# Kernel optimization log

Measured on AMD Instinct MI355X. Metric: run time of the kernel, lower is better.

The kernel has to match this reference:

```python
import jax, jax.numpy as jnp
import numpy as np


def gcn_conv(x, src, dst, W, b, num_nodes):
    # PyG GCNConv with add_self_loops=True, symmetric normalization.
    # src/dst already include self-loops.
    ones = jnp.ones(src.shape[0], dtype=x.dtype)
    deg = jax.ops.segment_sum(ones, dst, num_segments=num_nodes)  # [N]
    dinv = jnp.where(deg > 0, jax.lax.rsqrt(deg), 0.0)
    norm = dinv[src] * dinv[dst]                                   # [E+N]
    h = x @ W                                                      # [N, out]
    msg = h[src] * norm[:, None]                                   # gather + scale
    out = jax.ops.segment_sum(msg, dst, num_segments=num_nodes)    # scatter-add
    return out + b


def setup_inputs() -> dict:
    key = jax.random.key(0)
    k1, k2, k3, k4 = jax.random.split(key, 4)
    N, E = 50000, 1600000
    IN, HID, OUT = 1536, 256, 128
    x = jax.random.normal(k1, (N, IN), dtype=jnp.float32)
    edge_index = jax.random.randint(k2, (2, E), 0, N, dtype=jnp.int64)
    # Glorot-style scaled weights
    W1 = jax.random.normal(k3, (IN, HID), dtype=jnp.float32) / np.sqrt(IN)
    W2 = jax.random.normal(k4, (HID, OUT), dtype=jnp.float32) / np.sqrt(HID)
    b1 = jnp.zeros((HID,), dtype=jnp.float32)
    b2 = jnp.zeros((OUT,), dtype=jnp.float32)
    return {"x": x, "edge_index": edge_index, "W1": W1, "b1": b1,
            "W2": W2, "b2": b2, "num_nodes": N}


def reference(x, edge_index, W1, b1, W2, b2, num_nodes):
    loop = jnp.arange(num_nodes, dtype=edge_index.dtype)
    src = jnp.concatenate([edge_index[0], loop])
    dst = jnp.concatenate([edge_index[1], loop])
    h = gcn_conv(x, src, dst, W1, b1, num_nodes)
    h = jax.nn.relu(h)
    h = gcn_conv(h, src, dst, W2, b2, num_nodes)
    # F.normalize(h, dim=1): x / max(||x||_2, 1e-12)
    nrm = jnp.linalg.norm(h, axis=1, keepdims=True)
    return h / jnp.maximum(nrm, 1e-12)
```

## Files before the change

kernel.cpp:

```cpp
#include <hip/hip_runtime.h>

typedef __attribute__((ext_vector_type(4))) float f32x4;
typedef __attribute__((ext_vector_type(2))) float f32x2;
typedef __attribute__((ext_vector_type(8))) short s16x8;

static __device__ __forceinline__ unsigned short f2bf(float f) {
  unsigned int u = __builtin_bit_cast(unsigned int, f);
  u += 0x7fffu + ((u >> 16) & 1u);
  return (unsigned short)(u >> 16);
}

__global__ void zero_k(int* p, int n) {
  int i = blockIdx.x * 256 + threadIdx.x;
  if (i < n) p[i] = 0;
}
__global__ void deg_count_k(const int* __restrict__ edges, int* cnt, int E) {
  int e = blockIdx.x * 256 + threadIdx.x;
  if (e < E) atomicAdd(&cnt[edges[E + e]], 1);
}
__global__ void dinv_k(const int* __restrict__ cnt, float* dinv, int N) {
  int i = blockIdx.x * 256 + threadIdx.x;
  if (i < N) dinv[i] = rsqrtf((float)(cnt[i] + 1));
}

__global__ __launch_bounds__(256) void scan1_k(const int* __restrict__ cnt,
                                               int* __restrict__ loc,
                                               int* __restrict__ bsum, int N) {
  int t = threadIdx.x;
  int i0 = blockIdx.x * 1024 + t * 4;
  int c[4];
#pragma unroll
  for (int j = 0; j < 4; ++j) c[j] = (i0 + j < N) ? cnt[i0 + j] : 0;
  int tsum = c[0] + c[1] + c[2] + c[3];
  int lane = t & 63, wv = t >> 6;
  int incl = tsum;
#pragma unroll
  for (int off = 1; off < 64; off <<= 1) {
    int u = __shfl_up(incl, off, 64);
    if (lane >= off) incl += u;
  }
  __shared__ int ws[4];
  if (lane == 63) ws[wv] = incl;
  __syncthreads();
  int wbase = 0;
  for (int w = 0; w < wv; ++w) wbase += ws[w];
  int run = wbase + incl - tsum;
#pragma unroll
  for (int j = 0; j < 4; ++j) {
    if (i0 + j < N) loc[i0 + j] = run;
    run += c[j];
  }
  if (t == 255) bsum[blockIdx.x] = wbase + incl;
}
__global__ void scan2_k(int* bsum, int nb) {
  int lane = threadIdx.x;
  int v = (lane < nb) ? bsum[lane] : 0;
  int incl = v;
#pragma unroll
  for (int off = 1; off < 64; off <<= 1) {
    int u = __shfl_up(incl, off, 64);
    if (lane >= off) incl += u;
  }
  if (lane < nb) bsum[lane] = incl - v;
}
__global__ void addoff_k(int* loc, const int* __restrict__ bsum, int N) {
  int i = blockIdx.x * 256 + threadIdx.x;
  if (i < N) loc[i] += bsum[i >> 10];
}
__global__ void fill_k(const int* __restrict__ edges, const int* __restrict__ row,
                       int* cursor, int* __restrict__ csr, int E) {
  int e = blockIdx.x * 256 + threadIdx.x;
  if (e < E) {
    int s = edges[e], d = edges[E + e];
    int pos = atomicAdd(&cursor[d], 1);
    csr[row[d] + pos] = s;
  }
}

__global__ void convw_k(const float* __restrict__ W, unsigned short* __restrict__ Wt, int K, int Nn) {
  int t = blockIdx.x * 256 + threadIdx.x;
  if (t < K * Nn) {
    int n = t / K;
    int k = t - n * K;
    Wt[n * K + k] = f2bf(W[(long long)k * Nn + n]);
  }
}

template <int KTOT, int NTOT>
__global__ __launch_bounds__(256, 2) void gemm_k(
    const float* __restrict__ A, const unsigned short* __restrict__ Bt,
    const float* __restrict__ dinv, float* __restrict__ outg, int M) {
  constexpr int BM = 128, BK = 32, LD = BK + 8;
  constexpr int STRIP = NTOT / 4;
  constexpr int NF = STRIP / 16;
  constexpr int CH = NTOT / 64;

  __shared__ unsigned short Asm_[BM * LD];
  __shared__ unsigned short Bsm_[NTOT * LD];

  const int tid = threadIdx.x;
  const int wave = tid >> 6;
  const int lane = tid & 63;
  const int fr = lane & 15;
  const int quad = lane >> 4;
  const int m0 = blockIdx.x * BM;

  f32x4 acc[8][NF];
#pragma unroll
  for (int i = 0; i < 8; ++i)
#pragma unroll
    for (int j = 0; j < NF; ++j) { f32x4 z = {0.f, 0.f, 0.f, 0.f}; acc[i][j] = z; }

  const int sr = tid >> 1;
  const int sc = (tid & 1) << 4;
  const bool arow_ok = (m0 + sr) < M;
  const float* arow = A + (long long)(m0 + sr) * KTOT;

  auto loadA = [&](int k0, float* va) {
    if (arow_ok) {
      const f32x4* p = (const f32x4*)(arow + k0 + sc);
      f32x4 v0 = p[0], v1 = p[1], v2 = p[2], v3 = p[3];
#pragma unroll
      for (int j = 0; j < 4; ++j) { va[j] = v0[j]; va[4 + j] = v1[j]; va[8 + j] = v2[j]; va[12 + j] = v3[j]; }
    } else {
#pragma unroll
      for (int j = 0; j < 16; ++j) va[j] = 0.0f;
    }
  };
  auto loadB = [&](int k0, s16x8* vb) {
#pragma unroll
    for (int c = 0; c < CH; ++c) {
      int ch = tid + c * 256;
      int br = ch >> 2;
      int bc = (ch & 3) << 3;
      vb[c] = *(const s16x8*)&Bt[(long long)br * KTOT + k0 + bc];
    }
  };

  float va[16];
  s16x8 vb[CH];
  loadA(0, va);
  loadB(0, vb);

  for (int k0 = 0; k0 < KTOT; k0 += BK) {
    s16x8 h0, h1;
#pragma unroll
    for (int j = 0; j < 8; ++j) { h0[j] = (short)f2bf(va[j]); h1[j] = (short)f2bf(va[8 + j]); }

    __syncthreads();
    *(s16x8*)&Asm_[sr * LD + sc] = h0;
    *(s16x8*)&Asm_[sr * LD + sc + 8] = h1;
#pragma unroll
    for (int c = 0; c < CH; ++c) {
      int ch = tid + c * 256;
      int br = ch >> 2;
      int bc = (ch & 3) << 3;
      *(s16x8*)&Bsm_[br * LD + bc] = vb[c];
    }
    __syncthreads();

    if (k0 + BK < KTOT) { loadA(k0 + BK, va); loadB(k0 + BK, vb); }

    s16x8 af[8], bfr[NF];
#pragma unroll
    for (int mi = 0; mi < 8; ++mi) af[mi] = *(const s16x8*)&Asm_[(mi * 16 + fr) * LD + quad * 8];
#pragma unroll
    for (int ni = 0; ni < NF; ++ni) bfr[ni] = *(const s16x8*)&Bsm_[(wave * STRIP + ni * 16 + fr) * LD + quad * 8];
#pragma unroll
    for (int mi = 0; mi < 8; ++mi)
#pragma unroll
      for (int ni = 0; ni < NF; ++ni)
        acc[mi][ni] = __builtin_amdgcn_mfma_f32_16x16x32_bf16(af[mi], bfr[ni], acc[mi][ni], 0, 0, 0);
  }

#pragma unroll
  for (int mi = 0; mi < 8; ++mi) {
    int mbase = mi * 16 + quad * 4;
#pragma unroll
    for (int r = 0; r < 4; ++r) {
      int gm = m0 + mbase + r;
      if (gm < M) {
        float dv = dinv[gm];
#pragma unroll
        for (int ni = 0; ni < NF; ++ni) {
          int col = wave * STRIP + ni * 16 + fr;
          outg[(long long)gm * NTOT + col] = acc[mi][ni][r] * dv;
        }
      }
    }
  }
}

__global__ __launch_bounds__(256) void agg1_k(const int* __restrict__ csr,
                                              const int* __restrict__ row,
                                              const int* __restrict__ cnt,
                                              const float* __restrict__ g,
                                              const float* __restrict__ bias,
                                              const float* __restrict__ dinv,
                                              float* __restrict__ h, int N) {
  int node = blockIdx.x * 4 + (threadIdx.x >> 6);
  if (node >= N) return;
  int lane = threadIdx.x & 63;
  int f0 = lane << 2;
  f32x4 s = *(const f32x4*)&g[(long long)node * 256 + f0];
  int start = row[node], len = cnt[node];
  int j = 0;
  for (; j + 4 <= len; j += 4) {
    int i0 = csr[start + j], i1 = csr[start + j + 1];
    int i2 = csr[start + j + 2], i3 = csr[start + j + 3];
    f32x4 v0 = *(const f32x4*)&g[(long long)i0 * 256 + f0];
    f32x4 v1 = *(const f32x4*)&g[(long long)i1 * 256 + f0];
    f32x4 v2 = *(const f32x4*)&g[(long long)i2 * 256 + f0];
    f32x4 v3 = *(const f32x4*)&g[(long long)i3 * 256 + f0];
    s += v0; s += v1; s += v2; s += v3;
  }
  for (; j < len; ++j) {
    int i0 = csr[start + j];
    s += *(const f32x4*)&g[(long long)i0 * 256 + f0];
  }
  float dv = dinv[node];
  f32x4 b = *(const f32x4*)&bias[f0];
  f32x4 o;
#pragma unroll
  for (int k = 0; k < 4; ++k) o[k] = fmaxf(0.0f, b[k] + dv * s[k]);
  *(f32x4*)&h[(long long)node * 256 + f0] = o;
}

__global__ __launch_bounds__(256) void agg2_k(const int* __restrict__ csr,
                                              const int* __restrict__ row,
                                              const int* __restrict__ cnt,
                                              const float* __restrict__ g,
                                              const float* __restrict__ b2,
                                              const float* __restrict__ dinv,
                                              float* __restrict__ out, int N) {
  int node = blockIdx.x * 4 + (threadIdx.x >> 6);
  if (node >= N) return;
  int lane = threadIdx.x & 63;
  int f0 = lane << 1;
  f32x2 s = *(const f32x2*)&g[(long long)node * 128 + f0];
  int start = row[node], len = cnt[node];
  int j = 0;
  for (; j + 4 <= len; j += 4) {
    int i0 = csr[start + j], i1 = csr[start + j + 1];
    int i2 = csr[start + j + 2], i3 = csr[start + j + 3];
    f32x2 v0 = *(const f32x2*)&g[(long long)i0 * 128 + f0];
    f32x2 v1 = *(const f32x2*)&g[(long long)i1 * 128 + f0];
    f32x2 v2 = *(const f32x2*)&g[(long long)i2 * 128 + f0];
    f32x2 v3 = *(const f32x2*)&g[(long long)i3 * 128 + f0];
    s += v0; s += v1; s += v2; s += v3;
  }
  for (; j < len; ++j) {
    int i0 = csr[start + j];
    s += *(const f32x2*)&g[(long long)i0 * 128 + f0];
  }
  float dv = dinv[node];
  f32x2 b = *(const f32x2*)&b2[f0];
  float x0 = b[0] + dv * s[0];
  float x1 = b[1] + dv * s[1];
  float ss = x0 * x0 + x1 * x1;
#pragma unroll
  for (int off = 32; off > 0; off >>= 1) ss += __shfl_xor(ss, off, 64);
  float inv = 1.0f / fmaxf(sqrtf(ss), 1e-12f);
  f32x2 o = {x0 * inv, x1 * inv};
  *(f32x2*)&out[(long long)node * 128 + f0] = o;
}

extern "C" void kernel_launch(void* const* d_in, const int* in_sizes, int n_in,
                              void* d_out, int out_size, void* d_ws, size_t ws_size,
                              hipStream_t stream) {
  const float* x = (const float*)d_in[0];
  const int* edges = (const int*)d_in[1];
  const float* W1 = (const float*)d_in[2];
  const float* b1 = (const float*)d_in[3];
  const float* W2 = (const float*)d_in[4];
  const float* b2 = (const float*)d_in[5];
  float* out = (float*)d_out;

  const int HID = in_sizes[3];
  const int OUT = in_sizes[5];
  const int IN = in_sizes[2] / HID;
  const int N = in_sizes[0] / IN;
  const int E = in_sizes[1] / 2;

  size_t off = 0;
  auto carve = [&](size_t bytes) {
    void* p = (char*)d_ws + off;
    off += (bytes + 255) & ~(size_t)255;
    return p;
  };
  int* cnt = (int*)carve((size_t)N * 4);
  int* cursor = (int*)carve((size_t)N * 4);
  int* row = (int*)carve((size_t)N * 4);
  int* bsum = (int*)carve(64 * 4);
  int* csr = (int*)carve((size_t)E * 4);
  float* dinv = (float*)carve((size_t)N * 4);
  unsigned short* W1t = (unsigned short*)carve((size_t)IN * HID * 2);
  unsigned short* W2t = (unsigned short*)carve((size_t)HID * OUT * 2);
  float* g1 = (float*)carve((size_t)N * HID * 4);
  float* acc1 = (float*)carve((size_t)N * HID * 4);
  float* g2 = (float*)carve((size_t)N * OUT * 4);
  (void)ws_size; (void)n_in; (void)out_size;

  const int nb = (N + 1023) / 1024;

  zero_k<<<(N + 255) / 256, 256, 0, stream>>>(cnt, N);
  zero_k<<<(N + 255) / 256, 256, 0, stream>>>(cursor, N);
  deg_count_k<<<(E + 255) / 256, 256, 0, stream>>>(edges, cnt, E);
  dinv_k<<<(N + 255) / 256, 256, 0, stream>>>(cnt, dinv, N);

  scan1_k<<<nb, 256, 0, stream>>>(cnt, row, bsum, N);
  scan2_k<<<1, 64, 0, stream>>>(bsum, nb);
  addoff_k<<<(N + 255) / 256, 256, 0, stream>>>(row, bsum, N);
  fill_k<<<(E + 255) / 256, 256, 0, stream>>>(edges, row, cursor, csr, E);

  convw_k<<<(IN * HID + 255) / 256, 256, 0, stream>>>(W1, W1t, IN, HID);
  convw_k<<<(HID * OUT + 255) / 256, 256, 0, stream>>>(W2, W2t, HID, OUT);

  int mtiles = (N + 127) / 128;
  gemm_k<1536, 256><<<mtiles, 256, 0, stream>>>(x, W1t, dinv, g1, N);
  agg1_k<<<(N + 3) / 4, 256, 0, stream>>>(csr, row, cnt, g1, b1, dinv, acc1, N);
  gemm_k<256, 128><<<mtiles, 256, 0, stream>>>(acc1, W2t, dinv, g2, N);
  agg2_k<<<(N + 3) / 4, 256, 0, stream>>>(csr, row, cnt, g2, b2, dinv, out, N);
}
```

Before: 981.4 us.

## Store intermediate GEMM outputs and hidden activations in bf16, deepen gather unroll

Intermediate buffers g1, acc1 and g2 change from fp32 to bf16. This halves the bytes moved by the random-gather aggregation kernels and by the second GEMM's A loads, which now read bf16 directly and skip the conversion. The aggregation loops are unrolled to 8 neighbors to keep more loads in flight. The cost is extra rounding of intermediates, which could affect accuracy tolerance.

```diff
diff --git a/kernel.cpp b/kernel.cpp
--- a/kernel.cpp
+++ b/kernel.cpp
@@ -3,11 +3,17 @@
 typedef __attribute__((ext_vector_type(4))) float f32x4;
 typedef __attribute__((ext_vector_type(2))) float f32x2;
 typedef __attribute__((ext_vector_type(8))) short s16x8;
+typedef __attribute__((ext_vector_type(4))) unsigned short u16x4;
+typedef __attribute__((ext_vector_type(2))) unsigned short u16x2;
 
 static __device__ __forceinline__ unsigned short f2bf(float f) {
   unsigned int u = __builtin_bit_cast(unsigned int, f);
   u += 0x7fffu + ((u >> 16) & 1u);
   return (unsigned short)(u >> 16);
+}
+static __device__ __forceinline__ float bf2f(unsigned short h) {
+  unsigned int u = ((unsigned int)h) << 16;
+  return __builtin_bit_cast(float, u);
 }
 
 __global__ void zero_k(int* p, int n) {
@@ -86,10 +92,10 @@
   }
 }
 
-template <int KTOT, int NTOT>
+template <int KTOT, int NTOT, bool A_BF16>
 __global__ __launch_bounds__(256, 2) void gemm_k(
-    const float* __restrict__ A, const unsigned short* __restrict__ Bt,
-    const float* __restrict__ dinv, float* __restrict__ outg, int M) {
+    const void* __restrict__ Aptr, const unsigned short* __restrict__ Bt,
+    const float* __restrict__ dinv, unsigned short* __restrict__ outg, int M) {
   constexpr int BM = 128, BK = 32, LD = BK + 8;
   constexpr int STRIP = NTOT / 4;
   constexpr int NF = STRIP / 16;
@@ -114,20 +120,35 @@
   const int sr = tid >> 1;
   const int sc = (tid & 1) << 4;
   const bool arow_ok = (m0 + sr) < M;
-  const float* arow = A + (long long)(m0 + sr) * KTOT;
-
-  auto loadA = [&](int k0, float* va) {
-    if (arow_ok) {
-      const f32x4* p = (const f32x4*)(arow + k0 + sc);
-      f32x4 v0 = p[0], v1 = p[1], v2 = p[2], v3 = p[3];
-#pragma unroll
-      for (int j = 0; j < 4; ++j) { va[j] = v0[j]; va[4 + j] = v1[j]; va[8 + j] = v2[j]; va[12 + j] = v3[j]; }
+  const float* arowf = (const float*)Aptr + (long long)(m0 + sr) * KTOT;
+  const unsigned short* arowh = (const unsigned short*)Aptr + (long long)(m0 + sr) * KTOT;
+
+  float va[16];
+  s16x8 vah[2];
+
+  auto loadA = [&](int k0) {
+    if constexpr (A_BF16) {
+      if (arow_ok) {
+        vah[0] = *(const s16x8*)(arowh + k0 + sc);
+        vah[1] = *(const s16x8*)(arowh + k0 + sc + 8);
+      } else {
+        s16x8 z = {0, 0, 0, 0, 0, 0, 0, 0};
+        vah[0] = z; vah[1] = z;
+      }
     } else {
-#pragma unroll
-      for (int j = 0; j < 16; ++j) va[j] = 0.0f;
+      if (arow_ok) {
+        const f32x4* p = (const f32x4*)(arowf + k0 + sc);
+        f32x4 v0 = p[0], v1 = p[1], v2 = p[2], v3 = p[3];
+#pragma unroll
+        for (int j = 0; j < 4; ++j) { va[j] = v0[j]; va[4 + j] = v1[j]; va[8 + j] = v2[j]; va[12 + j] = v3[j]; }
+      } else {
+#pragma unroll
+        for (int j = 0; j < 16; ++j) va[j] = 0.0f;
+      }
     }
   };
-  auto loadB = [&](int k0, s16x8* vb) {
+  s16x8 vb[CH];
+  auto loadB = [&](int k0) {
 #pragma unroll
     for (int c = 0; c < CH; ++c) {
       int ch = tid + c * 256;
@@ -137,15 +158,20 @@
     }
   };
 
-  float va[16];
-  s16x8 vb[CH];
-  loadA(0, va);
-  loadB(0, vb);
+  loadA(0);
+  loadB(0);
 
   for (int k0 = 0; k0 < KTOT; k0 += BK) {
     s16x8 h0, h1;
-#pragma unroll
-    for (int j = 0; j < 8; ++j) { h0[j] = (short)f2bf(va[j]); h1[j] = (short)f2bf(va[8 + j]); }
+    if constexpr (A_BF16) {
+      h0 = vah[0]; h1 = vah[1];
+    } else {
+#pragma unroll
+      for (int j = 0; j < 8; ++j) { h0[j] = (short)f2bf(va[j]); h1[j] = (short)f2bf(va[8 + j]); }
+    }
+    s16x8 vbc[CH];
+#pragma unroll
+    for (int c = 0; c < CH; ++c) vbc[c] = vb[c];
 
     __syncthreads();
     *(s16x8*)&Asm_[sr * LD + sc] = h0;
@@ -155,11 +181,11 @@
       int ch = tid + c * 256;
       int br = ch >> 2;
       int bc = (ch & 3) << 3;
-      *(s16x8*)&Bsm_[br * LD + bc] = vb[c];
+      *(s16x8*)&Bsm_[br * LD + bc] = vbc[c];
     }
     __syncthreads();
 
-    if (k0 + BK < KTOT) { loadA(k0 + BK, va); loadB(k0 + BK, vb); }
+    if (k0 + BK < KTOT) { loadA(k0 + BK); loadB(k0 + BK); }
 
     s16x8 af[8], bfr[NF];
 #pragma unroll
@@ -184,7 +210,7 @@
 #pragma unroll
         for (int ni = 0; ni < NF; ++ni) {
           int col = wave * STRIP + ni * 16 + fr;
-          outg[(long long)gm * NTOT + col] = acc[mi][ni][r] * dv;
+          outg[(long long)gm * NTOT + col] = f2bf(acc[mi][ni][r] * dv);
         }
       }
     }
@@ -194,42 +220,48 @@
 __global__ __launch_bounds__(256) void agg1_k(const int* __restrict__ csr,
                                               const int* __restrict__ row,
                                               const int* __restrict__ cnt,
-                                              const float* __restrict__ g,
+                                              const unsigned short* __restrict__ g,
                                               const float* __restrict__ bias,
                                               const float* __restrict__ dinv,
-                                              float* __restrict__ h, int N) {
+                                              unsigned short* __restrict__ h, int N) {
   int node = blockIdx.x * 4 + (threadIdx.x >> 6);
   if (node >= N) return;
   int lane = threadIdx.x & 63;
   int f0 = lane << 2;
-  f32x4 s = *(const f32x4*)&g[(long long)node * 256 + f0];
+  u16x4 sv = *(const u16x4*)&g[(long long)node * 256 + f0];
+  f32x4 s = {bf2f(sv[0]), bf2f(sv[1]), bf2f(sv[2]), bf2f(sv[3])};
   int start = row[node], len = cnt[node];
   int j = 0;
-  for (; j + 4 <= len; j += 4) {
-    int i0 = csr[start + j], i1 = csr[start + j + 1];
-    int i2 = csr[start + j + 2], i3 = csr[start + j + 3];
-    f32x4 v0 = *(const f32x4*)&g[(long long)i0 * 256 + f0];
-    f32x4 v1 = *(const f32x4*)&g[(long long)i1 * 256 + f0];
-    f32x4 v2 = *(const f32x4*)&g[(long long)i2 * 256 + f0];
-    f32x4 v3 = *(const f32x4*)&g[(long long)i3 * 256 + f0];
-    s += v0; s += v1; s += v2; s += v3;
+  for (; j + 8 <= len; j += 8) {
+    int idx[8];
+#pragma unroll
+    for (int t = 0; t < 8; ++t) idx[t] = csr[start + j + t];
+    u16x4 v[8];
+#pragma unroll
+    for (int t = 0; t < 8; ++t) v[t] = *(const u16x4*)&g[(long long)idx[t] * 256 + f0];
+#pragma unroll
+    for (int t = 0; t < 8; ++t) {
+      s[0] += bf2f(v[t][0]); s[1] += bf2f(v[t][1]);
+      s[2] += bf2f(v[t][2]); s[3] += bf2f(v[t][3]);
+    }
   }
   for (; j < len; ++j) {
     int i0 = csr[start + j];
-    s += *(const f32x4*)&g[(long long)i0 * 256 + f0];
+    u16x4 v = *(const u16x4*)&g[(long long)i0 * 256 + f0];
+    s[0] += bf2f(v[0]); s[1] += bf2f(v[1]); s[2] += bf2f(v[2]); s[3] += bf2f(v[3]);
   }
   float dv = dinv[node];
   f32x4 b = *(const f32x4*)&bias[f0];
-  f32x4 o;
-#pragma unroll
-  for (int k = 0; k < 4; ++k) o[k] = fmaxf(0.0f, b[k] + dv * s[k]);
-  *(f32x4*)&h[(long long)node * 256 + f0] = o;
+  u16x4 o;
+#pragma unroll
+  for (int k = 0; k < 4; ++k) o[k] = f2bf(fmaxf(0.0f, b[k] + dv * s[k]));
+  *(u16x4*)&h[(long long)node * 256 + f0] = o;
 }
 
 __global__ __launch_bounds__(256) void agg2_k(const int* __restrict__ csr,
                                               const int* __restrict__ row,
                                               const int* __restrict__ cnt,
-                                              const float* __restrict__ g,
+                                              const unsigned short* __restrict__ g,
                                               const float* __restrict__ b2,
                                               const float* __restrict__ dinv,
                                               float* __restrict__ out, int N) {
@@ -237,26 +269,29 @@
   if (node >= N) return;
   int lane = threadIdx.x & 63;
   int f0 = lane << 1;
-  f32x2 s = *(const f32x2*)&g[(long long)node * 128 + f0];
+  u16x2 sv = *(const u16x2*)&g[(long long)node * 128 + f0];
+  float s0 = bf2f(sv[0]), s1 = bf2f(sv[1]);
   int start = row[node], len = cnt[node];
   int j = 0;
-  for (; j + 4 <= len; j += 4) {
-    int i0 = csr[start + j], i1 = csr[start + j + 1];
-    int i2 = csr[start + j + 2], i3 = csr[start + j + 3];
-    f32x2 v0 = *(const f32x2*)&g[(long long)i0 * 128 + f0];
-    f32x2 v1 = *(const f32x2*)&g[(long long)i1 * 128 + f0];
-    f32x2 v2 = *(const f32x2*)&g[(long long)i2 * 128 + f0];
-    f32x2 v3 = *(const f32x2*)&g[(long long)i3 * 128 + f0];
-    s += v0; s += v1; s += v2; s += v3;
+  for (; j + 8 <= len; j += 8) {
+    int idx[8];
+#pragma unroll
+    for (int t = 0; t < 8; ++t) idx[t] = csr[start + j + t];
+    u16x2 v[8];
+#pragma unroll
+    for (int t = 0; t < 8; ++t) v[t] = *(const u16x2*)&g[(long long)idx[t] * 128 + f0];
+#pragma unroll
+    for (int t = 0; t < 8; ++t) { s0 += bf2f(v[t][0]); s1 += bf2f(v[t][1]); }
   }
   for (; j < len; ++j) {
     int i0 = csr[start + j];
-    s += *(const f32x2*)&g[(long long)i0 * 128 + f0];
+    u16x2 v = *(const u16x2*)&g[(long long)i0 * 128 + f0];
+    s0 += bf2f(v[0]); s1 += bf2f(v[1]);
   }
   float dv = dinv[node];
   f32x2 b = *(const f32x2*)&b2[f0];
-  float x0 = b[0] + dv * s[0];
-  float x1 = b[1] + dv * s[1];
+  float x0 = b[0] + dv * s0;
+  float x1 = b[1] + dv * s1;
   float ss = x0 * x0 + x1 * x1;
 #pragma unroll
   for (int off = 32; off > 0; off >>= 1) ss += __shfl_xor(ss, off, 64);
@@ -296,9 +331,9 @@
   float* dinv = (float*)carve((size_t)N * 4);
   unsigned short* W1t = (unsigned short*)carve((size_t)IN * HID * 2);
   unsigned short* W2t = (unsigned short*)carve((size_t)HID * OUT * 2);
-  float* g1 = (float*)carve((size_t)N * HID * 4);
-  float* acc1 = (float*)carve((size_t)N * HID * 4);
-  float* g2 = (float*)carve((size_t)N * OUT * 4);
+  unsigned short* g1 = (unsigned short*)carve((size_t)N * HID * 2);
+  unsigned short* acc1 = (unsigned short*)carve((size_t)N * HID * 2);
+  unsigned short* g2 = (unsigned short*)carve((size_t)N * OUT * 2);
   (void)ws_size; (void)n_in; (void)out_size;
 
   const int nb = (N + 1023) / 1024;
@@ -317,8 +352,8 @@
   convw_k<<<(HID * OUT + 255) / 256, 256, 0, stream>>>(W2, W2t, HID, OUT);
 
   int mtiles = (N + 127) / 128;
-  gemm_k<1536, 256><<<mtiles, 256, 0, stream>>>(x, W1t, dinv, g1, N);
+  gemm_k<1536, 256, false><<<mtiles, 256, 0, stream>>>(x, W1t, dinv, g1, N);
   agg1_k<<<(N + 3) / 4, 256, 0, stream>>>(csr, row, cnt, g1, b1, dinv, acc1, N);
-  gemm_k<256, 128><<<mtiles, 256, 0, stream>>>(acc1, W2t, dinv, g2, N);
+  gemm_k<256, 128, true><<<mtiles, 256, 0, stream>>>(acc1, W2t, dinv, g2, N);
   agg2_k<<<(N + 3) / 4, 256, 0, stream>>>(csr, row, cnt, g2, b2, dinv, out, N);
 }
```

New measurement: 814.4 us. -17.0%, faster.
